# Kernel tuning notes

Hardware: AMD Instinct MI355X
Metric: run time of the kernel (lower is better)

The kernel has to match this reference:

```python
import jax, jax.numpy as jnp
import numpy as np

BLOCK = 32  # GGML Q8_0 block size: 32 int8 values share one scale


def setup_inputs() -> dict:
    key = jax.random.key(0)
    k1, k2, k3 = jax.random.split(key, 3)
    B, S, I, O = 2, 2048, 4096, 4096
    A = jax.random.normal(k1, (B, S, I), dtype=jnp.float32)
    # quantized weight values: stored unsigned 0..255, interpreted as signed (v - 128)
    w_q = jax.random.randint(k2, (O, I), 0, 255, dtype=jnp.int32)
    # one scale per block of 32 along infeatures
    scales = jax.random.uniform(k3, (O, I // BLOCK), dtype=jnp.float32) * 0.05
    return {"A": A, "w_q": w_q, "scales": scales}


def reference(A, w_q, scales):
    # Fused dequant + matmul (GGML Q8_0-style):
    # W[o, i] = (w_q[o, i] - 128) * scales[o, i // 32]
    O, I = w_q.shape
    q = w_q.astype(jnp.float32) - 128.0                      # [O, I]
    W = (q.reshape(O, I // BLOCK, BLOCK) * scales[:, :, None]).reshape(O, I)
    # C = A @ W^T, matching ggml mul_mat (weight is [outfeatures, infeatures])
    return jnp.einsum('bsi,oi->bso', A, W)
```

## Files before the change

### kernel.cpp

```cpp
#include <hip/hip_runtime.h>
#include <stdint.h>

typedef unsigned short u16;
typedef __bf16 bf16x8 __attribute__((ext_vector_type(8)));
typedef float f32x4 __attribute__((ext_vector_type(4)));
typedef unsigned short u16x8 __attribute__((ext_vector_type(8)));

__device__ __forceinline__ u16 f2bf(float f) {
  union { float f; uint32_t u; } x; x.f = f;
  uint32_t r = x.u + 0x7fffu + ((x.u >> 16) & 1u);
  return (u16)(r >> 16);
}

__global__ __launch_bounds__(256) void cvt_all(
    const float* __restrict__ A, u16* __restrict__ Ab, size_t n8a,
    const int* __restrict__ Wq, const float* __restrict__ S,
    u16* __restrict__ Wb, size_t n8w) {
  size_t i = (size_t)blockIdx.x * 256 + threadIdx.x;
  if (i < n8a) {
    const float4* p = (const float4*)(A + i * 8);
    float4 v0 = p[0], v1 = p[1];
    u16x8 r = { f2bf(v0.x), f2bf(v0.y), f2bf(v0.z), f2bf(v0.w),
                f2bf(v1.x), f2bf(v1.y), f2bf(v1.z), f2bf(v1.w) };
    *(u16x8*)(Ab + i * 8) = r;
  } else {
    size_t j = i - n8a;
    if (j >= n8w) return;
    const int4* p = (const int4*)(Wq + j * 8);
    int4 v0 = p[0], v1 = p[1];
    float s = S[j >> 2];
    u16x8 r = { f2bf((float)(v0.x - 128) * s), f2bf((float)(v0.y - 128) * s),
                f2bf((float)(v0.z - 128) * s), f2bf((float)(v0.w - 128) * s),
                f2bf((float)(v1.x - 128) * s), f2bf((float)(v1.y - 128) * s),
                f2bf((float)(v1.z - 128) * s), f2bf((float)(v1.w - 128) * s) };
    *(u16x8*)(Wb + j * 8) = r;
  }
}

__device__ __forceinline__ void load_lds_16B(const void* g, void* l) {
  __builtin_amdgcn_global_load_lds(
      (const __attribute__((address_space(1))) unsigned int*)g,
      (__attribute__((address_space(3))) unsigned int*)l, 16, 0, 0);
}

#define BM 256
#define BN 256
#define BK 64

#define BAR()    __builtin_amdgcn_s_barrier()
#define VMBAR(N) asm volatile("s_waitcnt vmcnt(" #N ")\n\ts_barrier" ::: "memory")

__global__ __launch_bounds__(512) void gemm8(
    const u16* __restrict__ Ab, const u16* __restrict__ Wb,
    float* __restrict__ C, int M, int N, int K) {
  __shared__ u16 As[2][BM * BK];
  __shared__ u16 Bs[2][BN * BK];

  const int NT = K >> 6;
  const int K2 = K * 2;
  const int tid = (int)threadIdx.x;
  const int lane = tid & 63;
  const int wvu = __builtin_amdgcn_readfirstlane(tid >> 6);
  const int wm = wvu >> 2, wn = wvu & 3;
  const int lrow = lane & 15, lq = lane >> 4;

  const int nbx = N / BN;
  const int cpx = (int)gridDim.x >> 3;
  const int swz = ((int)blockIdx.x & 7) * cpx + ((int)blockIdx.x >> 3);
  const int m0 = (swz / nbx) * BM, n0 = (swz % nbx) * BN;

  const int srow = lane >> 3, schunk = (lane & 7) ^ srow;
  const uint32_t voff = (uint32_t)srow * (uint32_t)K2 + (uint32_t)schunk * 16;
  const char* baseA = (const char*)(Ab + (size_t)m0 * K);
  const char* baseB = (const char*)(Wb + (size_t)n0 * K);

  const int sx = lrow & 7;
  int offA[2], offB[2];
  #pragma unroll
  for (int ks = 0; ks < 2; ++ks) {
    const int slot = ((ks * 4 + lq) ^ sx) * 8;
    offA[ks] = (wm * 128 + lrow) * BK + slot;
    offB[ks] = (wn * 64 + lrow) * BK + slot;
  }

#define STAGE_A(BUF, MH, KT) do { \
    _Pragma("unroll") \
    for (int it = 0; it < 2; ++it) { \
      const int o = wvu * 2 + it; \
      const int rb = o * 8 + (o >> 3) * 64 + (MH) * 64; \
      load_lds_16B(baseA + (size_t)rb * K2 + (size_t)(KT) * 128 + voff, \
                   (char*)&As[BUF][0] + rb * 128); \
    } } while (0)

#define STAGE_B(BUF, NH, KT) do { \
    _Pragma("unroll") \
    for (int it = 0; it < 2; ++it) { \
      const int o = wvu * 2 + it; \
      const int rb = (o >> 2) * 64 + (o & 3) * 8 + (NH) * 32; \
      load_lds_16B(baseB + (size_t)rb * K2 + (size_t)(KT) * 128 + voff, \
                   (char*)&Bs[BUF][0] + rb * 128); \
    } } while (0)

#define LDA(DST, BUF, MH) do { \
    _Pragma("unroll") \
    for (int ii = 0; ii < 4; ++ii) \
      _Pragma("unroll") \
      for (int ks = 0; ks < 2; ++ks) \
        DST[ii][ks] = *(const bf16x8*)((const u16*)As + \
            ((BUF) * (BM * BK) + ((MH) * 64 + ii * 16) * BK) + offA[ks]); \
  } while (0)

#define LDB(DST, BUF, NH) do { \
    _Pragma("unroll") \
    for (int jj = 0; jj < 2; ++jj) \
      _Pragma("unroll") \
      for (int ks = 0; ks < 2; ++ks) \
        DST[jj][ks] = *(const bf16x8*)((const u16*)Bs + \
            ((BUF) * (BN * BK) + ((NH) * 32 + jj * 16) * BK) + offB[ks]); \
  } while (0)

#define QUAD(MH, NH, ASET, BSET) do { \
    __builtin_amdgcn_s_setprio(1); \
    _Pragma("unroll") \
    for (int ii = 0; ii < 4; ++ii) \
      _Pragma("unroll") \
      for (int jj = 0; jj < 2; ++jj) { \
        acc[(MH)*4+ii][(NH)*2+jj] = __builtin_amdgcn_mfma_f32_16x16x32_bf16( \
            ASET[ii][0], BSET[jj][0], acc[(MH)*4+ii][(NH)*2+jj], 0, 0, 0); \
        acc[(MH)*4+ii][(NH)*2+jj] = __builtin_amdgcn_mfma_f32_16x16x32_bf16( \
            ASET[ii][1], BSET[jj][1], acc[(MH)*4+ii][(NH)*2+jj], 0, 0, 0); \
      } \
    __builtin_amdgcn_s_setprio(0); \
  } while (0)

  f32x4 acc[8][4] = {};
  bf16x8 a0[4][2], a1[4][2], b0[2][2], b1[2][2];

  STAGE_B(0, 0, 0); STAGE_A(0, 0, 0); STAGE_A(0, 1, 0); STAGE_B(0, 1, 0);
  STAGE_B(1, 0, 1); STAGE_A(1, 0, 1); STAGE_A(1, 1, 1); STAGE_B(1, 1, 1);
  VMBAR(8);
  LDA(a0, 0, 0); LDB(b0, 0, 0);

#define HALF(T, BUF, NBUF) do { \
     \
    LDA(a1, BUF, 1); \
    BAR(); \
    QUAD(0, 0, a0, b0); \
    BAR(); \
     \
    LDB(b1, BUF, 1); \
    STAGE_B(BUF, 0, (T) + 2); \
    BAR(); \
    QUAD(1, 0, a1, b0); \
    BAR(); \
     \
    STAGE_A(BUF, 0, (T) + 2); \
    BAR(); \
    QUAD(0, 1, a0, b1); \
    BAR(); \
     \
    STAGE_A(BUF, 1, (T) + 2); \
    STAGE_B(BUF, 1, (T) + 2); \
    VMBAR(8); \
    LDA(a0, NBUF, 0); LDB(b0, NBUF, 0); \
    QUAD(1, 1, a1, b1); \
    BAR(); \
  } while (0)

#define HALF_T1(BUF, NBUF) do { \
    LDA(a1, BUF, 1); \
    BAR(); QUAD(0, 0, a0, b0); BAR(); \
    LDB(b1, BUF, 1); \
    BAR(); QUAD(1, 0, a1, b0); BAR(); \
    BAR(); QUAD(0, 1, a0, b1); BAR(); \
    VMBAR(0); \
    LDA(a0, NBUF, 0); LDB(b0, NBUF, 0); \
    QUAD(1, 1, a1, b1); \
    BAR(); \
  } while (0)

#define HALF_T2(BUF) do { \
    LDA(a1, BUF, 1); \
    BAR(); QUAD(0, 0, a0, b0); BAR(); \
    LDB(b1, BUF, 1); \
    BAR(); QUAD(1, 0, a1, b0); BAR(); \
    BAR(); QUAD(0, 1, a0, b1); BAR(); \
    QUAD(1, 1, a1, b1); \
  } while (0)

  int t = 0;
  for (; t + 3 < NT; t += 2) {
    HALF(t, 0, 1);
    HALF(t + 1, 1, 0);
  }
  HALF_T1(0, 1);
  HALF_T2(1);

  #pragma unroll
  for (int i = 0; i < 8; ++i)
    #pragma unroll
    for (int r = 0; r < 4; ++r) {
      const int gm = m0 + wm * 128 + i * 16 + lq * 4 + r;
      float* crow = C + (size_t)gm * N + n0 + wn * 64 + lrow;
      #pragma unroll
      for (int j = 0; j < 4; ++j) crow[j * 16] = acc[i][j][r];
    }

#undef HALF_T2
#undef HALF_T1
#undef HALF
#undef QUAD
#undef LDB
#undef LDA
#undef STAGE_B
#undef STAGE_A
}

#define FBM 256
#define FBN 128
#define FBK 32

template <int MODE>
__global__ __launch_bounds__(256, 2) void gemm_fb(
    const u16* __restrict__ Ab, const u16* __restrict__ Wb,
    const float* __restrict__ Af, const int* __restrict__ Wq,
    const float* __restrict__ Sc, float* __restrict__ C,
    int M, int N, int K) {
  __shared__ u16 As[FBM * FBK];
  __shared__ u16 Bs[FBN * FBK];

  const int tid = threadIdx.x;
  const int wave = tid >> 6, lane = tid & 63;
  const int m0 = blockIdx.y * FBM, n0 = blockIdx.x * FBN;
  const int wm = (wave & 1) * 128, wn = (wave >> 1) * 64;
  const int lrow = lane & 15, lq = lane >> 4;

  const u16* gB[2]; u16* dB[2];
  if constexpr (MODE <= 1) {
    #pragma unroll
    for (int it = 0; it < 2; ++it) {
      int q = wave * 128 + it * 64 + lane;
      int row = q >> 2, s = q & 3;
      int c = (s - (row >> 1)) & 3;
      gB[it] = Wb + (size_t)(n0 + row) * K + c * 8;
      dB[it] = Bs + (size_t)(wave * 128 + it * 64) * 8;
    }
  }

  const u16* fA[8]; const u16* fB[4];
  #pragma unroll
  for (int i = 0; i < 8; ++i) {
    int row = wm + i * 16 + lrow;
    int s = (lq + (row >> 1)) & 3;
    fA[i] = As + row * FBK + s * 8;
  }
  #pragma unroll
  for (int j = 0; j < 4; ++j) {
    int row = wn + j * 16 + lrow;
    int s = (lq + (row >> 1)) & 3;
    fB[j] = Bs + row * FBK + s * 8;
  }

  f32x4 acc[8][4] = {};

  for (int k0 = 0; k0 < K; k0 += FBK) {
    #pragma unroll
    for (int it = 0; it < 4; ++it) {
      int g = it * 256 + tid;
      int row = g >> 2, c8 = g & 3;
      int s = (c8 + (row >> 1)) & 3;
      const float4* p = (const float4*)(Af + (size_t)(m0 + row) * K + k0 + c8 * 8);
      float4 v0 = p[0], v1 = p[1];
      u16x8 r = { f2bf(v0.x), f2bf(v0.y), f2bf(v0.z), f2bf(v0.w),
                  f2bf(v1.x), f2bf(v1.y), f2bf(v1.z), f2bf(v1.w) };
      *(u16x8*)(As + row * FBK + s * 8) = r;
    }
    if constexpr (MODE == 1) {
      #pragma unroll
      for (int it = 0; it < 2; ++it) load_lds_16B(gB[it] + k0, dB[it]);
    } else {
      #pragma unroll
      for (int it = 0; it < 2; ++it) {
        int g = it * 256 + tid;
        int row = g >> 2, c8 = g & 3;
        int s = (c8 + (row >> 1)) & 3;
        const int4* p = (const int4*)(Wq + (size_t)(n0 + row) * K + k0 + c8 * 8);
        int4 v0 = p[0], v1 = p[1];
        float sc = Sc[(size_t)(n0 + row) * (K >> 5) + (k0 >> 5)];
        u16x8 r = { f2bf((float)(v0.x - 128) * sc), f2bf((float)(v0.y - 128) * sc),
                    f2bf((float)(v0.z - 128) * sc), f2bf((float)(v0.w - 128) * sc),
                    f2bf((float)(v1.x - 128) * sc), f2bf((float)(v1.y - 128) * sc),
                    f2bf((float)(v1.z - 128) * sc), f2bf((float)(v1.w - 128) * sc) };
        *(u16x8*)(Bs + row * FBK + s * 8) = r;
      }
    }
    __syncthreads();

    bf16x8 a[8], b[4];
    #pragma unroll
    for (int i = 0; i < 8; ++i) a[i] = *(const bf16x8*)fA[i];
    #pragma unroll
    for (int j = 0; j < 4; ++j) b[j] = *(const bf16x8*)fB[j];
    #pragma unroll
    for (int i = 0; i < 8; ++i)
      #pragma unroll
      for (int j = 0; j < 4; ++j)
        acc[i][j] = __builtin_amdgcn_mfma_f32_16x16x32_bf16(a[i], b[j], acc[i][j], 0, 0, 0);
    __syncthreads();
  }

  #pragma unroll
  for (int i = 0; i < 8; ++i) {
    #pragma unroll
    for (int r = 0; r < 4; ++r) {
      int gm = m0 + wm + i * 16 + lq * 4 + r;
      float* crow = C + (size_t)gm * N + n0 + wn + lrow;
      #pragma unroll
      for (int j = 0; j < 4; ++j) crow[j * 16] = acc[i][j][r];
    }
  }
}

extern "C" void kernel_launch(void* const* d_in, const int* in_sizes, int n_in,
                              void* d_out, int out_size, void* d_ws, size_t ws_size,
                              hipStream_t stream) {
  const float* A  = (const float*)d_in[0];
  const int*   Wq = (const int*)d_in[1];
  const float* S  = (const float*)d_in[2];
  float* C = (float*)d_out;

  const int K = 4096;
  const int N = in_sizes[1] / K;
  const int M = in_sizes[0] / K;

  const size_t needA = (size_t)M * K * sizeof(u16);
  const size_t needW = (size_t)N * K * sizeof(u16);

  if (ws_size >= needA + needW) {
    u16* Ab = (u16*)d_ws;
    u16* Wb = (u16*)((char*)d_ws + needA);
    size_t nA8 = (size_t)M * K / 8, nW8 = (size_t)N * K / 8;
    cvt_all<<<(int)((nA8 + nW8 + 255) / 256), 256, 0, stream>>>(A, Ab, nA8, Wq, S, Wb, nW8);
    gemm8<<<dim3((M / BM) * (N / BN)), dim3(512), 0, stream>>>(Ab, Wb, C, M, N, K);
  } else if (ws_size >= needW) {
    u16* Wb = (u16*)d_ws;
    size_t nW8 = (size_t)N * K / 8;
    cvt_all<<<(int)((nW8 + 255) / 256), 256, 0, stream>>>(nullptr, nullptr, 0, Wq, S, Wb, nW8);
    gemm_fb<1><<<dim3(N / FBN, M / FBM), dim3(256), 0, stream>>>(nullptr, Wb, A, nullptr, nullptr, C, M, N, K);
  } else {
    gemm_fb<2><<<dim3(N / FBN, M / FBM), dim3(256), 0, stream>>>(nullptr, nullptr, A, Wq, S, C, M, N, K);
  }
}
```

Measured before the change: 285.8 us.

## Restructure GEMM main loop pipeline to cut barriers and reorder LDS stages

Reworks the double-buffered main loop schedule. The first register loads of each tile now happen at the start of each half-iteration, and the last B staging of the next buffer is deferred into the loop. The number of block barriers per half-iteration drops from about seven to three, and the vmcnt wait threshold goes from 8 to 6. The goal is less synchronisation stall and more overlap of global-to-LDS staging with MFMA work. In exchange, correctness now depends on subtle LDS read/write ordering with fewer barriers, which risks races.

```diff
diff --git a/kernel.cpp b/kernel.cpp
--- a/kernel.cpp
+++ b/kernel.cpp
@@ -137,54 +137,52 @@
   bf16x8 a0[4][2], a1[4][2], b0[2][2], b1[2][2];
 
   STAGE_B(0, 0, 0); STAGE_A(0, 0, 0); STAGE_A(0, 1, 0); STAGE_B(0, 1, 0);
-  STAGE_B(1, 0, 1); STAGE_A(1, 0, 1); STAGE_A(1, 1, 1); STAGE_B(1, 1, 1);
-  VMBAR(8);
-  LDA(a0, 0, 0); LDB(b0, 0, 0);
+  STAGE_B(1, 0, 1); STAGE_A(1, 0, 1); STAGE_A(1, 1, 1);
+  VMBAR(6);
 
 #define HALF(T, BUF, NBUF) do { \
-     \
+    LDA(a0, BUF, 0); LDB(b0, BUF, 0); \
+    STAGE_B(NBUF, 1, (T) + 1); \
+    BAR(); \
+    QUAD(0, 0, a0, b0); \
     LDA(a1, BUF, 1); \
     BAR(); \
-    QUAD(0, 0, a0, b0); \
-    BAR(); \
-     \
+    QUAD(1, 0, a1, b0); \
     LDB(b1, BUF, 1); \
     STAGE_B(BUF, 0, (T) + 2); \
     BAR(); \
+    QUAD(0, 1, a0, b1); \
+    STAGE_A(BUF, 0, (T) + 2); \
+    STAGE_A(BUF, 1, (T) + 2); \
+    VMBAR(6); \
+    QUAD(1, 1, a1, b1); \
+  } while (0)
+
+#define HALF_T1(T, BUF, NBUF) do { \
+    LDA(a0, BUF, 0); LDB(b0, BUF, 0); \
+    STAGE_B(NBUF, 1, (T) + 1); \
+    BAR(); \
+    QUAD(0, 0, a0, b0); \
+    LDA(a1, BUF, 1); \
+    BAR(); \
     QUAD(1, 0, a1, b0); \
-    BAR(); \
-     \
-    STAGE_A(BUF, 0, (T) + 2); \
+    LDB(b1, BUF, 1); \
     BAR(); \
     QUAD(0, 1, a0, b1); \
-    BAR(); \
-     \
-    STAGE_A(BUF, 1, (T) + 2); \
-    STAGE_B(BUF, 1, (T) + 2); \
-    VMBAR(8); \
-    LDA(a0, NBUF, 0); LDB(b0, NBUF, 0); \
+    VMBAR(0); \
     QUAD(1, 1, a1, b1); \
-    BAR(); \
-  } while (0)
-
-#define HALF_T1(BUF, NBUF) do { \
+  } while (0)
+
+#define HALF_T2(BUF) do { \
+    LDA(a0, BUF, 0); LDB(b0, BUF, 0); \
+    BAR(); \
+    QUAD(0, 0, a0, b0); \
     LDA(a1, BUF, 1); \
-    BAR(); QUAD(0, 0, a0, b0); BAR(); \
+    BAR(); \
+    QUAD(1, 0, a1, b0); \
     LDB(b1, BUF, 1); \
-    BAR(); QUAD(1, 0, a1, b0); BAR(); \
-    BAR(); QUAD(0, 1, a0, b1); BAR(); \
-    VMBAR(0); \
-    LDA(a0, NBUF, 0); LDB(b0, NBUF, 0); \
-    QUAD(1, 1, a1, b1); \
-    BAR(); \
-  } while (0)
-
-#define HALF_T2(BUF) do { \
-    LDA(a1, BUF, 1); \
-    BAR(); QUAD(0, 0, a0, b0); BAR(); \
-    LDB(b1, BUF, 1); \
-    BAR(); QUAD(1, 0, a1, b0); BAR(); \
-    BAR(); QUAD(0, 1, a0, b1); BAR(); \
+    BAR(); \
+    QUAD(0, 1, a0, b1); \
     QUAD(1, 1, a1, b1); \
   } while (0)
 
@@ -193,7 +191,7 @@
     HALF(t, 0, 1);
     HALF(t + 1, 1, 0);
   }
-  HALF_T1(0, 1);
+  HALF_T1(t, 0, 1);
   HALF_T2(1);
 
   #pragma unroll
```

Result: faster. 276.2 us (-3.4%).
